# Kernel optimization log

Hardware: AMD Instinct MI355X
Metric: run time of the kernel (lower is better)

The kernel has to match this reference:

```python
import jax, jax.numpy as jnp
import numpy as np

K = 4
TEMP = 0.5
PAD = 1

def setup_inputs() -> dict:
    key = jax.random.key(0)
    ks = jax.random.split(key, 5)
    B, C, H, W = 32, 256, 64, 64
    O, HID = 256, 65  # int(256*0.25)+1
    x = jax.random.normal(ks[0], (B, C, H, W), dtype=jnp.float32)
    w1 = jax.random.normal(ks[1], (HID, C), dtype=jnp.float32) * 0.05
    w2 = jax.random.normal(ks[2], (K * O, HID), dtype=jnp.float32) * 0.05
    b2 = jnp.zeros((K * O,), dtype=jnp.float32)
    weight = jax.random.normal(ks[3], (K, O, C, 3, 3), dtype=jnp.float32) * 0.05
    return {"x": x, "w1": w1, "w2": w2, "b2": b2, "weight": weight}

def _dyn_conv(x, w1, w2, b2, weight):
    B, C, H, W = x.shape
    Kk, O = weight.shape[0], weight.shape[1]
    # GPM2d attention: global avg pool -> 1x1 conv -> relu -> 1x1 conv -> softmax over K
    pooled = jnp.mean(x, axis=(2, 3))                     # [B, C]
    h = jax.nn.relu(pooled @ w1.T)                        # [B, HID]
    logits = (h @ w2.T + b2).reshape(B, Kk, O)            # [B, K, O]
    attn = jax.nn.softmax(logits / TEMP, axis=1)          # softmax over K experts
    # aggregate per-sample, per-out-channel weights: [B, O, C, k, k]
    agg_w = jnp.einsum('bko,kocij->bocij', attn, weight)
    # per-sample conv (equivalent to groups=batch trick in torch)
    def conv1(xi, wi):
        return jax.lax.conv_general_dilated(
            xi[None], wi, window_strides=(1, 1),
            padding=[(PAD, PAD), (PAD, PAD)],
            dimension_numbers=('NCHW', 'OIHW', 'NCHW'))[0]
    return jax.vmap(conv1)(x, agg_w)                      # [B, O, H, W]

def reference(x, w1, w2, b2, weight):
    return _dyn_conv(x, w1, w2, b2, weight)
```

## Files before the change

kernel.cpp:

```cpp
#include <hip/hip_runtime.h>
#include <stdint.h>

typedef unsigned short ushort_t;
typedef __attribute__((ext_vector_type(8))) short short8;
typedef __attribute__((ext_vector_type(8))) unsigned short ushortx8;
typedef __attribute__((ext_vector_type(4))) float floatx4;

#define B_    32
#define C_    256
#define O_    256
#define HID_  65
#define HW_   4096
#define KDIM  2304
#define XP_H  66
#define XPAD_ELEMS ((size_t)B_ * XP_H * XP_H * C_)
#define WAGG_ELEMS ((size_t)B_ * O_ * KDIM)

static __device__ __forceinline__ unsigned short f2bf(float f) {
  unsigned u = __float_as_uint(f);
  u += 0x7fffu + ((u >> 16) & 1u);
  return (unsigned short)(u >> 16);
}

static __device__ __forceinline__ void gld_lds16(const void* g, void* l) {
  __builtin_amdgcn_global_load_lds((__attribute__((address_space(1))) void*)(g),
                                   (__attribute__((address_space(3))) void*)(l),
                                   16, 0, 0);
}

__global__ void pad_kernel(const float* __restrict__ x, ushort_t* __restrict__ xpad,
                           float* __restrict__ partial) {
  __shared__ float tileT[64][65];
  __shared__ float pool[4][64];
  const int hwT = blockIdx.x, cT = blockIdx.y, b = blockIdx.z;
  const int t = threadIdx.x;
  const int hw0 = hwT * 64, c0 = cT * 64;
  const float* src = x + ((size_t)(b * C_ + c0)) * HW_ + hw0;

  if (cT == 0) {
    const int tid = hwT * 256 + t;
    if (tid < 8320) {
      uint4 z = {0u, 0u, 0u, 0u};
      uint4* base = (uint4*)(xpad + (size_t)b * XP_H * XP_H * C_);
      size_t idx;
      if (tid < 2112) idx = (size_t)tid;
      else if (tid < 4224) idx = (size_t)65 * 2112 + (tid - 2112);
      else if (tid < 6272) {
        const int i = tid - 4224;
        idx = (size_t)(1 + (i >> 5)) * 2112 + (i & 31);
      } else {
        const int i = tid - 6272;
        idx = (size_t)(1 + (i >> 5)) * 2112 + 65 * 32 + (i & 31);
      }
      base[idx] = z;
    }
  }

#pragma unroll
  for (int p = 0; p < 4; ++p) {
    const int flat = p * 256 + t;
    const int c = flat >> 4, h4 = (flat & 15) * 4;
    const float4 v = *(const float4*)(src + (size_t)c * HW_ + h4);
    tileT[h4 + 0][c] = v.x;
    tileT[h4 + 1][c] = v.y;
    tileT[h4 + 2][c] = v.z;
    tileT[h4 + 3][c] = v.w;
  }
  __syncthreads();

  {
    const int c = t & 63, qh = t >> 6;
    float s = 0.f;
#pragma unroll
    for (int i = 0; i < 16; ++i) s += tileT[qh * 16 + i][c];
    pool[qh][c] = s;
  }
  __syncthreads();
  if (t < 64) {
    partial[(size_t)hwT * (B_ * C_) + b * C_ + c0 + t] =
        pool[0][t] + pool[1][t] + pool[2][t] + pool[3][t];
  }

#pragma unroll
  for (int p = 0; p < 2; ++p) {
    const int flat = p * 256 + t;
    const int hw = flat >> 3, cg = (flat & 7) * 8;
    ushortx8 v;
#pragma unroll
    for (int j = 0; j < 8; ++j) v[j] = f2bf(tileT[hw][cg + j]);
    const int h = (hw0 + hw) >> 6, w = (hw0 + hw) & 63;
    *(ushortx8*)(xpad + (((size_t)b * XP_H + (h + 1)) * XP_H + (w + 1)) * C_ + c0 + cg) = v;
  }
}

__global__ void attn_kernel(const float* __restrict__ partial,
                            const float* __restrict__ w1,
                            const float* __restrict__ w2,
                            const float* __restrict__ b2,
                            float* __restrict__ attn) {
  __shared__ float sp[C_];
  __shared__ float sh[HID_];
  const int b = blockIdx.x, t = threadIdx.x;
  {
    float s = 0.f;
#pragma unroll
    for (int i = 0; i < 64; ++i) s += partial[(size_t)i * (B_ * C_) + b * C_ + t];
    sp[t] = s * (1.f / 4096.f);
  }
  __syncthreads();
  if (t < HID_) {
    float a = 0.f;
    for (int c = 0; c < C_; ++c) a += sp[c] * w1[t * C_ + c];
    sh[t] = fmaxf(a, 0.f);
  }
  __syncthreads();
  float lg[4];
#pragma unroll
  for (int k = 0; k < 4; ++k) {
    float a = b2[k * O_ + t];
    for (int j = 0; j < HID_; ++j) a += sh[j] * w2[(k * O_ + t) * HID_ + j];
    lg[k] = a * 2.0f;
  }
  float mx = fmaxf(fmaxf(lg[0], lg[1]), fmaxf(lg[2], lg[3]));
  float e0 = expf(lg[0] - mx), e1 = expf(lg[1] - mx);
  float e2 = expf(lg[2] - mx), e3 = expf(lg[3] - mx);
  float inv = 1.f / (e0 + e1 + e2 + e3);
  attn[(b * 4 + 0) * O_ + t] = e0 * inv;
  attn[(b * 4 + 1) * O_ + t] = e1 * inv;
  attn[(b * 4 + 2) * O_ + t] = e2 * inv;
  attn[(b * 4 + 3) * O_ + t] = e3 * inv;
}

__global__ void agg_kernel(const float* __restrict__ attn,
                           const float* __restrict__ wt,
                           ushort_t* __restrict__ wagg) {
  const int o = blockIdx.x;
  const int b0 = blockIdx.y * 4;
  const int t = threadIdx.x;
  float wr[4][9];
#pragma unroll
  for (int k = 0; k < 4; ++k) {
    const float* src = wt + (size_t)(k * O_ + o) * KDIM + t * 9;
#pragma unroll
    for (int n = 0; n < 9; ++n) wr[k][n] = src[n];
  }
#pragma unroll
  for (int bi = 0; bi < 4; ++bi) {
    const int b = b0 + bi;
    const float a0 = attn[(b * 4 + 0) * O_ + o];
    const float a1 = attn[(b * 4 + 1) * O_ + o];
    const float a2 = attn[(b * 4 + 2) * O_ + o];
    const float a3 = attn[(b * 4 + 3) * O_ + o];
    ushort_t* dst = wagg + (size_t)(b * O_ + o) * KDIM;
#pragma unroll
    for (int n = 0; n < 9; ++n) {
      float v = a0 * wr[0][n] + a1 * wr[1][n] + a2 * wr[2][n] + a3 * wr[3][n];
      dst[n * C_ + t] = f2bf(v);
    }
  }
}

__global__ __launch_bounds__(256) void gemm_kernel(const ushort_t* __restrict__ xpad,
                                                   const ushort_t* __restrict__ wagg,
                                                   float* __restrict__ out) {
  __shared__ short lA[128 * 64];
  __shared__ short lB[128 * 64];

  const int bid = blockIdx.x;
  const int xcd = bid & 7;
  const int q   = bid >> 3;
  const int b   = xcd + ((q >> 6) << 3);
  const int oT  = (q >> 5) & 1;
  const int hwT = q & 31;

  const int t    = threadIdx.x;
  const int lane = t & 63;
  const int wv   = t >> 6;

  const int hwBase = hwT << 7;
  const int h0     = hwT << 1;
  const int oBase  = oT << 7;

  const int rS = lane >> 3;
  const int pS = lane & 7;
  size_t aG[4], bG[4];
  int ldsOff[4];
#pragma unroll
  for (int qq = 0; qq < 4; ++qq) {
    const int row = wv * 32 + qq * 8 + rS;
    const int lch = pS ^ (row & 7);
    aG[qq] = (size_t)(b * O_ + oBase + row) * KDIM + lch * 8;
    const int hl = row >> 6, wl2 = row & 63;
    bG[qq] = ((size_t)(b * XP_H + h0 + hl) * XP_H + wl2) * C_ + lch * 8;
    ldsOff[qq] = (wv * 32 + qq * 8) * 64;
  }

  const int lm   = lane & 15;
  const int quad = lane >> 4;
  const int mW = (wv & 1) << 6;
  const int nW = (wv >> 1) << 6;
  int aOff[2][4], bOff[2][4];
#pragma unroll
  for (int h = 0; h < 2; ++h)
#pragma unroll
    for (int i = 0; i < 4; ++i) {
      const int ps = ((h * 4 + quad) ^ (lm & 7)) * 8;
      aOff[h][i] = (mW + i * 16 + lm) * 64 + ps;
      bOff[h][i] = (nW + i * 16 + lm) * 64 + ps;
    }

  floatx4 acc[4][4] = {};

  for (int tap = 0; tap < 9; ++tap) {
    const int toff = (tap / 3) * XP_H + (tap % 3);
#pragma unroll 1
    for (int c0 = 0; c0 < C_; c0 += 64) {
      const int kk = tap * C_ + c0;
      __syncthreads();
#pragma unroll
      for (int qq = 0; qq < 4; ++qq) {
        gld_lds16(wagg + aG[qq] + kk, lA + ldsOff[qq]);
        gld_lds16(xpad + bG[qq] + (size_t)toff * C_ + c0, lB + ldsOff[qq]);
      }
      __builtin_amdgcn_s_waitcnt(0x0f70);
      __syncthreads();

#pragma unroll
      for (int h = 0; h < 2; ++h) {
        short8 af[4], bf[4];
#pragma unroll
        for (int i = 0; i < 4; ++i) af[i] = *(const short8*)(lA + aOff[h][i]);
#pragma unroll
        for (int i = 0; i < 4; ++i) bf[i] = *(const short8*)(lB + bOff[h][i]);
#pragma unroll
        for (int mi = 0; mi < 4; ++mi)
#pragma unroll
          for (int ni = 0; ni < 4; ++ni)
            acc[mi][ni] = __builtin_amdgcn_mfma_f32_16x16x32_bf16(
                af[mi], bf[ni], acc[mi][ni], 0, 0, 0);
      }
    }
  }

  const size_t outBase = (size_t)b * O_ * HW_;
#pragma unroll
  for (int mi = 0; mi < 4; ++mi) {
#pragma unroll
    for (int ni = 0; ni < 4; ++ni) {
      const int hw = hwBase + nW + ni * 16 + lm;
#pragma unroll
      for (int r = 0; r < 4; ++r) {
        const int o = oBase + mW + mi * 16 + quad * 4 + r;
        out[outBase + (size_t)o * HW_ + hw] = acc[mi][ni][r];
      }
    }
  }
}

extern "C" void kernel_launch(void* const* d_in, const int* in_sizes, int n_in,
                              void* d_out, int out_size, void* d_ws, size_t ws_size,
                              hipStream_t stream) {
  const float* x  = (const float*)d_in[0];
  const float* w1 = (const float*)d_in[1];
  const float* w2 = (const float*)d_in[2];
  const float* b2 = (const float*)d_in[3];
  const float* wt = (const float*)d_in[4];
  float* out = (float*)d_out;

  char* ws = (char*)d_ws;
  ushort_t* xpad = (ushort_t*)ws;
  ushort_t* wagg = (ushort_t*)(ws + XPAD_ELEMS * 2);
  float* partial = (float*)(ws + XPAD_ELEMS * 2 + WAGG_ELEMS * 2);
  float* attn    = partial + 64 * B_ * C_;

  pad_kernel<<<dim3(64, 4, B_), 256, 0, stream>>>(x, xpad, partial);
  attn_kernel<<<B_, 256, 0, stream>>>(partial, w1, w2, b2, attn);
  agg_kernel<<<dim3(O_, 8), 256, 0, stream>>>(attn, wt, wagg);
  gemm_kernel<<<2048, 256, 0, stream>>>(xpad, wagg, out);
}
```

Before: 432.9 us.

## Use 256x256 tiles with 512 threads and double-buffered LDS prefetch in GEMM

The implicit-GEMM conv kernel moves from 128x128 tiles with 256 threads to 256x256 tiles with 512 threads (8 waves, each computing 128x64). The K loop over 9 taps x 4 channel chunks is flattened into 36 steps, and LDS is double-buffered so loads for step t+2 are issued while step t computes. It also adds setprio around the MFMA blocks. The aim is to cut global reloads and hide load latency. In exchange it uses 128KB of LDS and many accumulator registers per block, which lowers occupancy, and launches only 512 blocks.

```diff
diff --git a/kernel.cpp b/kernel.cpp
--- a/kernel.cpp
+++ b/kernel.cpp
@@ -160,97 +160,121 @@
   }
 }
 
-__global__ __launch_bounds__(256) void gemm_kernel(const ushort_t* __restrict__ xpad,
+__global__ __launch_bounds__(512) void gemm_kernel(const ushort_t* __restrict__ xpad,
                                                    const ushort_t* __restrict__ wagg,
                                                    float* __restrict__ out) {
-  __shared__ short lA[128 * 64];
-  __shared__ short lB[128 * 64];
+  __shared__ short lA0[2 * 256 * 64];
+  __shared__ short lB0[2 * 256 * 64];
 
   const int bid = blockIdx.x;
   const int xcd = bid & 7;
   const int q   = bid >> 3;
-  const int b   = xcd + ((q >> 6) << 3);
-  const int oT  = (q >> 5) & 1;
-  const int hwT = q & 31;
+  const int b   = xcd + ((q >> 4) << 3);
+  const int hwT = q & 15;
+  const int hwBase = hwT << 8;
+  const int h0     = hwT << 2;
 
   const int t    = threadIdx.x;
   const int lane = t & 63;
   const int wv   = t >> 6;
 
-  const int hwBase = hwT << 7;
-  const int h0     = hwT << 1;
-  const int oBase  = oT << 7;
-
-  const int rS = lane >> 3;
-  const int pS = lane & 7;
+  const int rS  = lane >> 3;
+  const int pS  = lane & 7;
+  const int lch = pS ^ rS;
   size_t aG[4], bG[4];
   int ldsOff[4];
 #pragma unroll
-  for (int qq = 0; qq < 4; ++qq) {
-    const int row = wv * 32 + qq * 8 + rS;
-    const int lch = pS ^ (row & 7);
-    aG[qq] = (size_t)(b * O_ + oBase + row) * KDIM + lch * 8;
+  for (int j = 0; j < 4; ++j) {
+    const int row = wv * 32 + j * 8 + rS;
+    aG[j] = (size_t)(b * O_ + row) * KDIM + lch * 8;
     const int hl = row >> 6, wl2 = row & 63;
-    bG[qq] = ((size_t)(b * XP_H + h0 + hl) * XP_H + wl2) * C_ + lch * 8;
-    ldsOff[qq] = (wv * 32 + qq * 8) * 64;
+    bG[j] = ((size_t)(b * XP_H + h0 + hl) * XP_H + wl2) * C_ + lch * 8;
+    ldsOff[j] = (wv * 32 + j * 8) * 64;
   }
 
   const int lm   = lane & 15;
   const int quad = lane >> 4;
-  const int mW = (wv & 1) << 6;
-  const int nW = (wv >> 1) << 6;
-  int aOff[2][4], bOff[2][4];
-#pragma unroll
-  for (int h = 0; h < 2; ++h)
-#pragma unroll
-    for (int i = 0; i < 4; ++i) {
-      const int ps = ((h * 4 + quad) ^ (lm & 7)) * 8;
-      aOff[h][i] = (mW + i * 16 + lm) * 64 + ps;
-      bOff[h][i] = (nW + i * 16 + lm) * 64 + ps;
-    }
-
-  floatx4 acc[4][4] = {};
-
-  for (int tap = 0; tap < 9; ++tap) {
-    const int toff = (tap / 3) * XP_H + (tap % 3);
+  const int wr   = wv >> 2;
+  const int wc   = wv & 3;
+  const int mW   = wr << 7;
+  const int nW   = wc << 6;
+  int aBase[2], bBase[2];
+#pragma unroll
+  for (int h = 0; h < 2; ++h) {
+    const int ps = ((h * 4 + quad) ^ (lm & 7)) * 8;
+    aBase[h] = (mW + lm) * 64 + ps;
+    bBase[h] = (nW + lm) * 64 + ps;
+  }
+
+  floatx4 acc[8][4] = {};
+
+#pragma unroll
+  for (int j = 0; j < 4; ++j) {
+    gld_lds16(wagg + aG[j], lA0 + ldsOff[j]);
+    gld_lds16(xpad + bG[j], lB0 + ldsOff[j]);
+  }
+#pragma unroll
+  for (int j = 0; j < 4; ++j) {
+    gld_lds16(wagg + aG[j] + 64, lA0 + 16384 + ldsOff[j]);
+    gld_lds16(xpad + bG[j] + 64, lB0 + 16384 + ldsOff[j]);
+  }
+  __builtin_amdgcn_s_waitcnt(0x0f78);
+  __builtin_amdgcn_s_barrier();
+  __builtin_amdgcn_sched_barrier(0);
+
 #pragma unroll 1
-    for (int c0 = 0; c0 < C_; c0 += 64) {
-      const int kk = tap * C_ + c0;
-      __syncthreads();
-#pragma unroll
-      for (int qq = 0; qq < 4; ++qq) {
-        gld_lds16(wagg + aG[qq] + kk, lA + ldsOff[qq]);
-        gld_lds16(xpad + bG[qq] + (size_t)toff * C_ + c0, lB + ldsOff[qq]);
+  for (int tt = 0; tt < 36; ++tt) {
+    const int cb = (tt & 1) * 16384;
+    const short* bufA = lA0 + cb;
+    const short* bufB = lB0 + cb;
+#pragma unroll
+    for (int h = 0; h < 2; ++h) {
+      short8 af[8], bf[4];
+#pragma unroll
+      for (int i = 0; i < 8; ++i) af[i] = *(const short8*)(bufA + aBase[h] + i * 1024);
+#pragma unroll
+      for (int i = 0; i < 4; ++i) bf[i] = *(const short8*)(bufB + bBase[h] + i * 1024);
+      __builtin_amdgcn_s_setprio(1);
+#pragma unroll
+      for (int mi = 0; mi < 8; ++mi)
+#pragma unroll
+        for (int ni = 0; ni < 4; ++ni)
+          acc[mi][ni] = __builtin_amdgcn_mfma_f32_16x16x32_bf16(
+              af[mi], bf[ni], acc[mi][ni], 0, 0, 0);
+      __builtin_amdgcn_s_setprio(0);
+    }
+    if (tt == 35) break;
+    __builtin_amdgcn_sched_barrier(0);
+    __builtin_amdgcn_s_barrier();
+    if (tt + 2 < 36) {
+      const int kt  = tt + 2;
+      const int tap = kt >> 2;
+      const size_t aK = (size_t)kt << 6;
+      const size_t bK = (size_t)((tap / 3) * XP_H + (tap % 3)) * C_ + ((kt & 3) << 6);
+      short* dA = lA0 + cb;
+      short* dB = lB0 + cb;
+#pragma unroll
+      for (int j = 0; j < 4; ++j) {
+        gld_lds16(wagg + aG[j] + aK, dA + ldsOff[j]);
+        gld_lds16(xpad + bG[j] + bK, dB + ldsOff[j]);
       }
+      __builtin_amdgcn_s_waitcnt(0x0f78);
+    } else {
       __builtin_amdgcn_s_waitcnt(0x0f70);
-      __syncthreads();
-
-#pragma unroll
-      for (int h = 0; h < 2; ++h) {
-        short8 af[4], bf[4];
-#pragma unroll
-        for (int i = 0; i < 4; ++i) af[i] = *(const short8*)(lA + aOff[h][i]);
-#pragma unroll
-        for (int i = 0; i < 4; ++i) bf[i] = *(const short8*)(lB + bOff[h][i]);
-#pragma unroll
-        for (int mi = 0; mi < 4; ++mi)
-#pragma unroll
-          for (int ni = 0; ni < 4; ++ni)
-            acc[mi][ni] = __builtin_amdgcn_mfma_f32_16x16x32_bf16(
-                af[mi], bf[ni], acc[mi][ni], 0, 0, 0);
-      }
-    }
+    }
+    __builtin_amdgcn_s_barrier();
+    __builtin_amdgcn_sched_barrier(0);
   }
 
   const size_t outBase = (size_t)b * O_ * HW_;
 #pragma unroll
-  for (int mi = 0; mi < 4; ++mi) {
+  for (int mi = 0; mi < 8; ++mi) {
 #pragma unroll
     for (int ni = 0; ni < 4; ++ni) {
       const int hw = hwBase + nW + ni * 16 + lm;
 #pragma unroll
       for (int r = 0; r < 4; ++r) {
-        const int o = oBase + mW + mi * 16 + quad * 4 + r;
+        const int o = mW + mi * 16 + quad * 4 + r;
         out[outBase + (size_t)o * HW_ + hw] = acc[mi][ni][r];
       }
     }
@@ -276,5 +300,5 @@
   pad_kernel<<<dim3(64, 4, B_), 256, 0, stream>>>(x, xpad, partial);
   attn_kernel<<<B_, 256, 0, stream>>>(partial, w1, w2, b2, attn);
   agg_kernel<<<dim3(O_, 8), 256, 0, stream>>>(attn, wt, wagg);
-  gemm_kernel<<<2048, 256, 0, stream>>>(xpad, wagg, out);
-}
+  gemm_kernel<<<512, 512, 0, stream>>>(xpad, wagg, out);
+}
```

New measurement: 428.5 us. About the same (-1.0%).
